# Optimization experiments

Measured on AMD Instinct MI355X. Metric: run time of the kernel, lower is better.

Reference implementation:

```python
import jax, jax.numpy as jnp
import numpy as np

N = 100000       # nodes
E = 1600000      # edges
DIM_IN = 128
DIM_H = 256
G = 512          # graphs in batch


def setup_inputs() -> dict:
    key = jax.random.key(0)
    ks = jax.random.split(key, 9)
    x = jax.random.normal(ks[0], (N, DIM_IN), dtype=jnp.float32)
    edge_index = jax.random.randint(ks[1], (2, E), 0, N, dtype=jnp.int32)
    batch = jnp.sort(jax.random.randint(ks[2], (N,), 0, G, dtype=jnp.int32))
    # GCNConv weights (glorot-ish scale) + biases, and linear head
    W1 = jax.random.normal(ks[3], (DIM_IN, DIM_H), dtype=jnp.float32) / np.sqrt(DIM_IN)
    b1 = jnp.zeros((DIM_H,), dtype=jnp.float32)
    W2 = jax.random.normal(ks[4], (DIM_H, DIM_H), dtype=jnp.float32) / np.sqrt(DIM_H)
    b2 = jnp.zeros((DIM_H,), dtype=jnp.float32)
    Wl = jax.random.normal(ks[5], (DIM_H, 1), dtype=jnp.float32) / np.sqrt(DIM_H)
    bl = jnp.zeros((1,), dtype=jnp.float32)
    return {"x": x, "edge_index": edge_index, "batch": batch,
            "W1": W1, "b1": b1, "W2": W2, "b2": b2, "Wl": Wl, "bl": bl}


def _gcn_conv(x, W, b, src, dst, norm):
    # PyG GCNConv: h = x @ W; message = norm_e * h[src]; aggregate at dst; + bias
    h = x @ W                                  # [N, d_out]
    msg = h[src] * norm[:, None]               # [E+N, d_out] edge-gathered
    out = jax.ops.segment_sum(msg, dst, num_segments=N)
    return out + b


def reference(x, edge_index, batch, W1, b1, W2, b2, Wl, bl):
    # add self-loops (PyG GCNConv default)
    loops = jnp.arange(N, dtype=edge_index.dtype)
    src = jnp.concatenate([edge_index[0], loops])   # [E+N]
    dst = jnp.concatenate([edge_index[1], loops])   # [E+N]
    # symmetric normalization: deg counted at dst (incl. self-loops)
    deg = jax.ops.segment_sum(jnp.ones_like(src, dtype=x.dtype), dst, num_segments=N)
    dinv = jax.lax.rsqrt(deg)                       # deg >= 1 due to self-loops
    norm = dinv[src] * dinv[dst]                    # [E+N]

    h = jax.nn.relu(_gcn_conv(x, W1, b1, src, dst, norm))
    h = jax.nn.relu(_gcn_conv(h, W2, b2, src, dst, norm))

    # global_mean_pool over graph ids
    sums = jax.ops.segment_sum(h, batch, num_segments=G)                  # [G, d]
    cnts = jax.ops.segment_sum(jnp.ones((N,), h.dtype), batch, num_segments=G)
    pooled = sums / jnp.maximum(cnts, 1.0)[:, None]

    return pooled @ Wl + bl                                              # [G, 1]
```

## Files before the change

kernel.cpp:

```cpp
#include <hip/hip_runtime.h>
#include <hip/hip_fp16.h>
#include <math.h>

typedef _Float16 f16x8 __attribute__((ext_vector_type(8)));
typedef float f32x4 __attribute__((ext_vector_type(4)));


__global__ void k_init(int* __restrict__ ecnt, int N) {
    int i = blockIdx.x * 256 + threadIdx.x;
    if (i < N) ecnt[i] = 0;
}

__global__ void k_edge_count(const int* __restrict__ dst, int* __restrict__ ecnt,
                             int* __restrict__ rank, int E) {
    int j = (blockIdx.x * 256 + threadIdx.x) * 2;
    if (j + 1 < E) {
        int2 d = *(const int2*)(dst + j);
        int r0 = atomicAdd(&ecnt[d.x], 1);
        int r1 = atomicAdd(&ecnt[d.y], 1);
        *(int2*)(rank + j) = make_int2(r0, r1);
    } else if (j < E) {
        rank[j] = atomicAdd(&ecnt[dst[j]], 1);
    }
}

__global__ void k_scanA(const int* __restrict__ ecnt, int* __restrict__ bsum, int N) {
    int t = threadIdx.x;
    int base = blockIdx.x * 1024;
    int s = 0;
#pragma unroll
    for (int j = 0; j < 4; ++j) {
        int i = base + j * 256 + t;
        if (i < N) s += ecnt[i];
    }
#pragma unroll
    for (int off = 32; off > 0; off >>= 1) s += __shfl_down(s, off, 64);
    __shared__ int wsum[4];
    if ((t & 63) == 0) wsum[t >> 6] = s;
    __syncthreads();
    if (t == 0) bsum[blockIdx.x] = wsum[0] + wsum[1] + wsum[2] + wsum[3];
}

__global__ void k_scanB(const int* __restrict__ bsum, int* __restrict__ boff, int NB,
                        int* __restrict__ rowstart, int N, int E) {
    __shared__ int sh[256];
    int t = threadIdx.x;
    int v = (t < NB) ? bsum[t] : 0;
    sh[t] = v;
    __syncthreads();
    for (int off = 1; off < 256; off <<= 1) {
        int u = (t >= off) ? sh[t - off] : 0;
        __syncthreads();
        sh[t] += u;
        __syncthreads();
    }
    if (t < NB) boff[t] = sh[t] - v;
    if (t == 0) rowstart[N] = E;
}

__global__ void k_scanC(const int* __restrict__ ecnt, const int* __restrict__ boff,
                        int* __restrict__ rowstart, float* __restrict__ dinv, int N) {
    int t = threadIdx.x;
    int base = blockIdx.x * 1024 + t * 4;
    int e[4];
    int s = 0;
#pragma unroll
    for (int j = 0; j < 4; ++j) {
        int i = base + j;
        e[j] = (i < N) ? ecnt[i] : 0;
        s += e[j];
    }
    __shared__ int sh[256];
    sh[t] = s;
    __syncthreads();
    for (int off = 1; off < 256; off <<= 1) {
        int u = (t >= off) ? sh[t - off] : 0;
        __syncthreads();
        sh[t] += u;
        __syncthreads();
    }
    int off0 = boff[blockIdx.x] + sh[t] - s;
    int run = 0;
#pragma unroll
    for (int j = 0; j < 4; ++j) {
        int i = base + j;
        if (i < N) {
            rowstart[i] = off0 + run;
            dinv[i] = rsqrtf((float)(e[j] + 1));
        }
        run += e[j];
    }
}

__global__ void k_scatter(const int* __restrict__ src, const int* __restrict__ dst,
                          const int* __restrict__ rowstart, const int* __restrict__ rank,
                          int* __restrict__ ssrc, int E) {
    int j = (blockIdx.x * 256 + threadIdx.x) * 4;
    if (j + 3 < E) {
        int4 s = *(const int4*)(src + j);
        int4 d = *(const int4*)(dst + j);
        int4 r = *(const int4*)(rank + j);
        ssrc[rowstart[d.x] + r.x] = s.x;
        ssrc[rowstart[d.y] + r.y] = s.y;
        ssrc[rowstart[d.z] + r.z] = s.z;
        ssrc[rowstart[d.w] + r.w] = s.w;
    } else {
        for (; j < E; ++j) ssrc[rowstart[dst[j]] + rank[j]] = src[j];
    }
}

__global__ void k_gstarts(const int* __restrict__ batch, int* __restrict__ gstart, int N, int G) {
    int i = blockIdx.x * 256 + threadIdx.x;
    if (i >= N) return;
    int bi = batch[i];
    int bp = (i == 0) ? -1 : batch[i - 1];
    for (int g = bp + 1; g <= bi; ++g) gstart[g] = i;
    if (i == N - 1) {
        for (int g = bi + 1; g <= G; ++g) gstart[g] = N;
    }
}


__global__ __launch_bounds__(256) void k_cast_f2h(const float* __restrict__ in,
                                                  __half* __restrict__ out, int n4) {
    int i = blockIdx.x * 256 + threadIdx.x;
    if (i >= n4) return;
    float4 v = *(const float4*)(in + (size_t)i * 4);
    __half2 a = __floats2half2_rn(v.x, v.y);
    __half2 b = __floats2half2_rn(v.z, v.w);
    union { __half2 h[2]; float2 f; } u;
    u.h[0] = a; u.h[1] = b;
    *(float2*)(out + (size_t)i * 4) = u.f;
}


__global__ __launch_bounds__(256) void k_wt_both(
    const float* __restrict__ W1, const float* __restrict__ W2,
    _Float16* __restrict__ W1t, _Float16* __restrict__ W2t) {
    int idx = blockIdx.x * 256 + threadIdx.x;
    if (idx < 128 * 256) {
        int c = idx >> 7, k = idx & 127;
        W1t[idx] = (_Float16)W1[k * 256 + c];
    } else if (idx < 128 * 256 + 256 * 256) {
        int j = idx - 128 * 256;
        int c = j >> 8, k = j & 255;
        W2t[j] = (_Float16)W2[k * 256 + c];
    }
}


__global__ __launch_bounds__(256) void k_agg_in(
    const _Float16* __restrict__ xh,
    const int* __restrict__ rowstart, const int* __restrict__ ssrc,
    const float* __restrict__ dinv, _Float16* __restrict__ xa_h, int N) {
    int qw = threadIdx.x >> 4;
    int l = threadIdx.x & 15;
    int v = blockIdx.x * 16 + qw;
    if (v >= N) return;
    float dv = dinv[v];
    float acc[8];
    {
        f16x8 s = *(const f16x8*)(xh + (size_t)v * 128 + l * 8);
#pragma unroll
        for (int j = 0; j < 8; ++j) acc[j] = (float)s[j] * dv;
    }
    int e = rowstart[v], e1 = rowstart[v + 1];
    for (; e + 4 <= e1; e += 4) {
        int u0 = ssrc[e], u1 = ssrc[e + 1], u2 = ssrc[e + 2], u3 = ssrc[e + 3];
        float d0 = dinv[u0], d1 = dinv[u1], d2 = dinv[u2], d3 = dinv[u3];
        f16x8 m0 = *(const f16x8*)(xh + (size_t)u0 * 128 + l * 8);
        f16x8 m1 = *(const f16x8*)(xh + (size_t)u1 * 128 + l * 8);
        f16x8 m2 = *(const f16x8*)(xh + (size_t)u2 * 128 + l * 8);
        f16x8 m3 = *(const f16x8*)(xh + (size_t)u3 * 128 + l * 8);
#pragma unroll
        for (int j = 0; j < 8; ++j) {
            acc[j] = fmaf((float)m0[j], d0, acc[j]);
            acc[j] = fmaf((float)m1[j], d1, acc[j]);
            acc[j] = fmaf((float)m2[j], d2, acc[j]);
            acc[j] = fmaf((float)m3[j], d3, acc[j]);
        }
    }
    for (; e < e1; ++e) {
        int u = ssrc[e];
        float d = dinv[u];
        f16x8 m = *(const f16x8*)(xh + (size_t)u * 128 + l * 8);
#pragma unroll
        for (int j = 0; j < 8; ++j) acc[j] = fmaf((float)m[j], d, acc[j]);
    }
    f16x8 o;
#pragma unroll
    for (int j = 0; j < 8; ++j) o[j] = (_Float16)(acc[j] * dv);
    *(f16x8*)(xa_h + (size_t)v * 128 + l * 8) = o;
}


__device__ __forceinline__ void acc_h4s(float4& acc, float2 raw) {
    union { float2 f; __half2 h[2]; } u;
    u.f = raw;
    float2 p0 = __half22float2(u.h[0]);
    float2 p1 = __half22float2(u.h[1]);
    acc.x += p0.x; acc.y += p0.y; acc.z += p1.x; acc.w += p1.y;
}

__global__ __launch_bounds__(256) void k_aggregate(
    const __half* __restrict__ hsh, const int* __restrict__ rowstart,
    const int* __restrict__ ssrc, const float* __restrict__ dinv,
    const float* __restrict__ bias, __half* __restrict__ h2h, int N) {
    int w = threadIdx.x >> 6;
    int l = threadIdx.x & 63;
    int v = blockIdx.x * 4 + w;
    if (v >= N) return;
    float4 acc = make_float4(0.f, 0.f, 0.f, 0.f);
    acc_h4s(acc, *(const float2*)(hsh + (size_t)v * 256 + l * 4));
    int e = rowstart[v], e1 = rowstart[v + 1];
    for (; e + 4 <= e1; e += 4) {
        int u0 = ssrc[e], u1 = ssrc[e + 1], u2 = ssrc[e + 2], u3 = ssrc[e + 3];
        float2 m0 = *(const float2*)(hsh + (size_t)u0 * 256 + l * 4);
        float2 m1 = *(const float2*)(hsh + (size_t)u1 * 256 + l * 4);
        float2 m2 = *(const float2*)(hsh + (size_t)u2 * 256 + l * 4);
        float2 m3 = *(const float2*)(hsh + (size_t)u3 * 256 + l * 4);
        acc_h4s(acc, m0);
        acc_h4s(acc, m1);
        acc_h4s(acc, m2);
        acc_h4s(acc, m3);
    }
    for (; e < e1; ++e) {
        int u = ssrc[e];
        acc_h4s(acc, *(const float2*)(hsh + (size_t)u * 256 + l * 4));
    }
    float d = dinv[v];
    float4 b = *(const float4*)(bias + l * 4);
    union { __half2 h[2]; float2 f; } uo;
    uo.h[0] = __floats2half2_rn(fmaxf(fmaf(acc.x, d, b.x), 0.f),
                                fmaxf(fmaf(acc.y, d, b.y), 0.f));
    uo.h[1] = __floats2half2_rn(fmaxf(fmaf(acc.z, d, b.z), 0.f),
                                fmaxf(fmaf(acc.w, d, b.w), 0.f));
    *(float2*)(h2h + (size_t)v * 256 + l * 4) = uo.f;
}


template<int K, int EPI>
__global__ __launch_bounds__(256, 2) void k_gemm_mfma(
    const _Float16* __restrict__ Ah, const _Float16* __restrict__ Wt,
    const float* __restrict__ dinv, const float* __restrict__ bias,
    _Float16* __restrict__ Ch, int Nrows, int nchunks) {
    constexpr int KS = K / 32;
    constexpr int RB = 2 * K;
    constexpr int NLD = 64 * RB / 4096;
    __shared__ _Float16 As[64 * K];

    int tid = threadIdx.x;
    int l = tid & 63;
    int wv = tid >> 6;

    int bc = wv * 64 + (l & 15);
    int bk = (l >> 4) * 8;
    f16x8 breg[4][KS];
#pragma unroll
    for (int ct = 0; ct < 4; ++ct)
#pragma unroll
        for (int ks = 0; ks < KS; ++ks)
            breg[ct][ks] = *(const f16x8*)(Wt + (size_t)(bc + ct * 16) * K + ks * 32 + bk);
    float bb[4];
    if (EPI == 1) {
#pragma unroll
        for (int ct = 0; ct < 4; ++ct) bb[ct] = bias[bc + ct * 16];
    }

    for (int ch = blockIdx.x; ch < nchunks; ch += gridDim.x) {
        int r0 = ch * 64;
#pragma unroll
        for (int i = 0; i < NLD; ++i) {
            int logical = i * 4096 + tid * 16;
            int row = logical / RB;
            int colb = (logical & (RB - 1)) ^ ((row & 7) << 4);
            int grow = r0 + row;
            grow = grow < Nrows ? grow : Nrows - 1;
            const char* src = (const char*)Ah + (size_t)grow * RB + colb;
            char* dst = (char*)As + i * 4096 + wv * 1024;
            __builtin_amdgcn_global_load_lds(
                (const __attribute__((address_space(1))) void*)src,
                (__attribute__((address_space(3))) void*)dst, 16, 0, 0);
        }
        __syncthreads();

#pragma unroll
        for (int rb = 0; rb < 4; ++rb) {
            f32x4 acc[4];
#pragma unroll
            for (int ct = 0; ct < 4; ++ct) acc[ct] = (f32x4){0.f, 0.f, 0.f, 0.f};
            int row = rb * 16 + (l & 15);
#pragma unroll
            for (int ks = 0; ks < KS; ++ks) {
                int lb = (row * RB + ks * 64 + (l >> 4) * 16) ^ ((l & 7) << 4);
                f16x8 a = *(const f16x8*)((const char*)As + lb);
#pragma unroll
                for (int ct = 0; ct < 4; ++ct)
                    acc[ct] = __builtin_amdgcn_mfma_f32_16x16x32_f16(a, breg[ct][ks], acc[ct], 0, 0, 0);
            }
            int rbase = r0 + rb * 16 + (l >> 4) * 4;
#pragma unroll
            for (int j = 0; j < 4; ++j) {
                int r = rbase + j;
                if (r < Nrows) {
                    if (EPI == 0) {
                        float sc = dinv[r];
#pragma unroll
                        for (int ct = 0; ct < 4; ++ct)
                            Ch[(size_t)r * 256 + bc + ct * 16] = (_Float16)(acc[ct][j] * sc);
                    } else {
#pragma unroll
                        for (int ct = 0; ct < 4; ++ct)
                            Ch[(size_t)r * 256 + bc + ct * 16] =
                                (_Float16)fmaxf(acc[ct][j] + bb[ct], 0.f);
                    }
                }
            }
        }
        __syncthreads();
    }
}


__global__ __launch_bounds__(256) void k_poolhead(
    const __half* __restrict__ h2h, const int* __restrict__ gstart,
    const float* __restrict__ Wl, const float* __restrict__ bl,
    float* __restrict__ out, int G) {
    int g = blockIdx.x;
    int t = threadIdx.x;
    int i0 = gstart[g], i1 = gstart[g + 1];
    float s = 0.f;
    for (int i = i0; i < i1; ++i) s += __half2float(h2h[(size_t)i * 256 + t]);
    float pooled = s / fmaxf((float)(i1 - i0), 1.f);
    float v = pooled * Wl[t];
#pragma unroll
    for (int off = 32; off > 0; off >>= 1) v += __shfl_down(v, off, 64);
    __shared__ float red[4];
    if ((t & 63) == 0) red[t >> 6] = v;
    __syncthreads();
    if (t == 0) out[g] = red[0] + red[1] + red[2] + red[3] + bl[0];
}


extern "C" void kernel_launch(void* const* d_in, const int* in_sizes, int n_in,
                              void* d_out, int out_size, void* d_ws, size_t ws_size,
                              hipStream_t stream) {
    const float* x  = (const float*)d_in[0];
    const int* ei   = (const int*)d_in[1];
    const int* batch= (const int*)d_in[2];
    const float* W1 = (const float*)d_in[3];
    const float* b1 = (const float*)d_in[4];
    const float* W2 = (const float*)d_in[5];
    const float* b2 = (const float*)d_in[6];
    const float* Wl = (const float*)d_in[7];
    const float* bl = (const float*)d_in[8];
    float* out = (float*)d_out;

    const int N = in_sizes[2];
    const int E = in_sizes[1] / 2;
    const int G = out_size;

    char* wsp = (char*)d_ws;
    size_t off = 0;
    auto carve = [&](size_t bytes) -> void* {
        void* p = wsp + off;
        off = (off + bytes + 255) & ~(size_t)255;
        return p;
    };
    float* bufA    = (float*)carve((size_t)N * 256 * 4);
    float* bufB    = (float*)carve((size_t)N * 256 * 4);
    float* dinv    = (float*)carve((size_t)N * 4);
    int* ecnt      = (int*)carve((size_t)N * 4);
    int* rowstart  = (int*)carve((size_t)(N + 1) * 4);
    int* rank      = (int*)carve((size_t)E * 4);
    int* ssrc      = (int*)carve((size_t)E * 4);
    const int NB = (N + 1023) / 1024;
    int* bsum      = (int*)carve((size_t)NB * 4);
    int* boff      = (int*)carve((size_t)NB * 4);
    int* gstart    = (int*)carve((size_t)(G + 1) * 4);
    _Float16* W1t  = (_Float16*)carve((size_t)256 * 128 * 2);
    _Float16* W2t  = (_Float16*)carve((size_t)256 * 256 * 2);
    (void)ws_size;

    _Float16* xh   = (_Float16*)bufA;
    _Float16* xa_h = (_Float16*)((char*)bufA + (size_t)N * 128 * 2);
    _Float16* h1h  = (_Float16*)((char*)bufA + (size_t)N * 128 * 4);
    _Float16* hsh  = (_Float16*)bufB;
    __half*   h2h  = (__half*)((char*)bufB + (size_t)N * 256 * 2);

    const int* esrc = ei;
    const int* edst = ei + E;

    int nb256 = (N + 255) / 256;
    int nchunks = (N + 63) / 64;

    hipLaunchKernelGGL(k_init, dim3(nb256), dim3(256), 0, stream, ecnt, N);
    hipLaunchKernelGGL(k_edge_count, dim3((E / 2 + 255) / 256), dim3(256), 0, stream,
                       edst, ecnt, rank, E);
    hipLaunchKernelGGL(k_scanA, dim3(NB), dim3(256), 0, stream, ecnt, bsum, N);
    hipLaunchKernelGGL(k_scanB, dim3(1), dim3(256), 0, stream, bsum, boff, NB, rowstart, N, E);
    hipLaunchKernelGGL(k_scanC, dim3(NB), dim3(256), 0, stream, ecnt, boff, rowstart, dinv, N);
    hipLaunchKernelGGL(k_scatter, dim3((E / 4 + 255) / 256), dim3(256), 0, stream,
                       esrc, edst, rowstart, rank, ssrc, E);
    hipLaunchKernelGGL(k_gstarts, dim3(nb256), dim3(256), 0, stream, batch, gstart, N, G);
    hipLaunchKernelGGL(k_cast_f2h, dim3((N * 32 + 255) / 256), dim3(256), 0, stream,
                       x, (__half*)xh, N * 32);
    hipLaunchKernelGGL(k_wt_both, dim3((128 * 256 + 256 * 256 + 255) / 256), dim3(256), 0, stream,
                       W1, W2, W1t, W2t);

    hipLaunchKernelGGL(k_agg_in, dim3((N + 15) / 16), dim3(256), 0, stream,
                       xh, rowstart, ssrc, dinv, xa_h, N);
    hipLaunchKernelGGL((k_gemm_mfma<128, 1>), dim3(512), dim3(256), 0, stream,
                       xa_h, W1t, (const float*)nullptr, b1, h1h, N, nchunks);
    hipLaunchKernelGGL((k_gemm_mfma<256, 0>), dim3(512), dim3(256), 0, stream,
                       h1h, W2t, dinv, (const float*)nullptr, hsh, N, nchunks);
    hipLaunchKernelGGL(k_aggregate, dim3((N + 3) / 4), dim3(256), 0, stream,
                       (const __half*)hsh, rowstart, ssrc, dinv, b2, h2h, N);
    hipLaunchKernelGGL(k_poolhead, dim3(G), dim3(256), 0, stream,
                       h2h, gstart, Wl, bl, out, G);
}
```

Before: 441.5 us.

## Fuse first-layer neighbor aggregation into GEMM1 and merge setup kernels

Neighbor aggregation for the input features is now computed directly into the GEMM's shared-memory tile, removing the intermediate aggregated buffer and its global write and read. The cast, transpose, degree-count zeroing and graph-start kernels are merged into one launch. The fused kernel runs the irregular gather inside a persistent grid of 512 blocks. This gives less latency hiding than the previous wide aggregation launch, and the GEMM phase now waits on gather completion.

```diff
diff --git a/kernel.cpp b/kernel.cpp
--- a/kernel.cpp
+++ b/kernel.cpp
@@ -5,11 +5,6 @@
 typedef _Float16 f16x8 __attribute__((ext_vector_type(8)));
 typedef float f32x4 __attribute__((ext_vector_type(4)));
 
-
-__global__ void k_init(int* __restrict__ ecnt, int N) {
-    int i = blockIdx.x * 256 + threadIdx.x;
-    if (i < N) ecnt[i] = 0;
-}
 
 __global__ void k_edge_count(const int* __restrict__ dst, int* __restrict__ ecnt,
                              int* __restrict__ rank, int E) {
@@ -109,88 +104,223 @@
     }
 }
 
-__global__ void k_gstarts(const int* __restrict__ batch, int* __restrict__ gstart, int N, int G) {
+
+__global__ __launch_bounds__(256) void k_misc(
+    const float* __restrict__ x, __half* __restrict__ xh,
+    const float* __restrict__ W1, const float* __restrict__ W2,
+    _Float16* __restrict__ W1t, _Float16* __restrict__ W2t,
+    const int* __restrict__ batch, int* __restrict__ gstart,
+    int* __restrict__ ecnt, int N, int G, int n4) {
     int i = blockIdx.x * 256 + threadIdx.x;
-    if (i >= N) return;
-    int bi = batch[i];
-    int bp = (i == 0) ? -1 : batch[i - 1];
-    for (int g = bp + 1; g <= bi; ++g) gstart[g] = i;
-    if (i == N - 1) {
-        for (int g = bi + 1; g <= G; ++g) gstart[g] = N;
-    }
-}
-
-
-__global__ __launch_bounds__(256) void k_cast_f2h(const float* __restrict__ in,
-                                                  __half* __restrict__ out, int n4) {
-    int i = blockIdx.x * 256 + threadIdx.x;
-    if (i >= n4) return;
-    float4 v = *(const float4*)(in + (size_t)i * 4);
-    __half2 a = __floats2half2_rn(v.x, v.y);
-    __half2 b = __floats2half2_rn(v.z, v.w);
-    union { __half2 h[2]; float2 f; } u;
-    u.h[0] = a; u.h[1] = b;
-    *(float2*)(out + (size_t)i * 4) = u.f;
-}
-
-
-__global__ __launch_bounds__(256) void k_wt_both(
-    const float* __restrict__ W1, const float* __restrict__ W2,
-    _Float16* __restrict__ W1t, _Float16* __restrict__ W2t) {
-    int idx = blockIdx.x * 256 + threadIdx.x;
-    if (idx < 128 * 256) {
-        int c = idx >> 7, k = idx & 127;
-        W1t[idx] = (_Float16)W1[k * 256 + c];
-    } else if (idx < 128 * 256 + 256 * 256) {
-        int j = idx - 128 * 256;
+    if (i < n4) {
+        float4 v = *(const float4*)(x + (size_t)i * 4);
+        union { __half2 h[2]; float2 f; } u;
+        u.h[0] = __floats2half2_rn(v.x, v.y);
+        u.h[1] = __floats2half2_rn(v.z, v.w);
+        *(float2*)(xh + (size_t)i * 4) = u.f;
+    }
+    if (i < N) {
+        ecnt[i] = 0;
+        int bi = batch[i];
+        int bp = (i == 0) ? -1 : batch[i - 1];
+        for (int g = bp + 1; g <= bi; ++g) gstart[g] = i;
+        if (i == N - 1) {
+            for (int g = bi + 1; g <= G; ++g) gstart[g] = N;
+        }
+    }
+    if (i < 128 * 256) {
+        int c = i >> 7, k = i & 127;
+        W1t[i] = (_Float16)W1[k * 256 + c];
+    } else if (i < 128 * 256 + 256 * 256) {
+        int j = i - 128 * 256;
         int c = j >> 8, k = j & 255;
         W2t[j] = (_Float16)W2[k * 256 + c];
     }
 }
 
 
-__global__ __launch_bounds__(256) void k_agg_in(
-    const _Float16* __restrict__ xh,
-    const int* __restrict__ rowstart, const int* __restrict__ ssrc,
-    const float* __restrict__ dinv, _Float16* __restrict__ xa_h, int N) {
-    int qw = threadIdx.x >> 4;
-    int l = threadIdx.x & 15;
-    int v = blockIdx.x * 16 + qw;
-    if (v >= N) return;
-    float dv = dinv[v];
-    float acc[8];
-    {
-        f16x8 s = *(const f16x8*)(xh + (size_t)v * 128 + l * 8);
-#pragma unroll
-        for (int j = 0; j < 8; ++j) acc[j] = (float)s[j] * dv;
-    }
-    int e = rowstart[v], e1 = rowstart[v + 1];
-    for (; e + 4 <= e1; e += 4) {
-        int u0 = ssrc[e], u1 = ssrc[e + 1], u2 = ssrc[e + 2], u3 = ssrc[e + 3];
-        float d0 = dinv[u0], d1 = dinv[u1], d2 = dinv[u2], d3 = dinv[u3];
-        f16x8 m0 = *(const f16x8*)(xh + (size_t)u0 * 128 + l * 8);
-        f16x8 m1 = *(const f16x8*)(xh + (size_t)u1 * 128 + l * 8);
-        f16x8 m2 = *(const f16x8*)(xh + (size_t)u2 * 128 + l * 8);
-        f16x8 m3 = *(const f16x8*)(xh + (size_t)u3 * 128 + l * 8);
-#pragma unroll
-        for (int j = 0; j < 8; ++j) {
-            acc[j] = fmaf((float)m0[j], d0, acc[j]);
-            acc[j] = fmaf((float)m1[j], d1, acc[j]);
-            acc[j] = fmaf((float)m2[j], d2, acc[j]);
-            acc[j] = fmaf((float)m3[j], d3, acc[j]);
-        }
-    }
-    for (; e < e1; ++e) {
-        int u = ssrc[e];
-        float d = dinv[u];
-        f16x8 m = *(const f16x8*)(xh + (size_t)u * 128 + l * 8);
-#pragma unroll
-        for (int j = 0; j < 8; ++j) acc[j] = fmaf((float)m[j], d, acc[j]);
-    }
-    f16x8 o;
-#pragma unroll
-    for (int j = 0; j < 8; ++j) o[j] = (_Float16)(acc[j] * dv);
-    *(f16x8*)(xa_h + (size_t)v * 128 + l * 8) = o;
+__global__ __launch_bounds__(256, 2) void k_agg_gemm1(
+    const _Float16* __restrict__ xh, const int* __restrict__ rowstart,
+    const int* __restrict__ ssrc, const float* __restrict__ dinv,
+    const float* __restrict__ bias, const _Float16* __restrict__ Wt,
+    _Float16* __restrict__ Ch, int Nrows, int nchunks) {
+    constexpr int K = 128, KS = K / 32, RB = 2 * K;
+    __shared__ _Float16 As[64 * K];
+
+    int tid = threadIdx.x;
+    int l = tid & 63;
+    int wv = tid >> 6;
+    int qw = tid >> 4, l16 = tid & 15;
+
+    int bc = wv * 64 + (l & 15);
+    int bk = (l >> 4) * 8;
+    f16x8 breg[4][KS];
+#pragma unroll
+    for (int ct = 0; ct < 4; ++ct)
+#pragma unroll
+        for (int ks = 0; ks < KS; ++ks)
+            breg[ct][ks] = *(const f16x8*)(Wt + (size_t)(bc + ct * 16) * K + ks * 32 + bk);
+    float bb[4];
+#pragma unroll
+    for (int ct = 0; ct < 4; ++ct) bb[ct] = bias[bc + ct * 16];
+
+    for (int ch = blockIdx.x; ch < nchunks; ch += gridDim.x) {
+        int r0 = ch * 64;
+#pragma unroll
+        for (int round = 0; round < 4; ++round) {
+            int row = round * 16 + qw;
+            int v = r0 + row;
+            float acc[8] = {0.f, 0.f, 0.f, 0.f, 0.f, 0.f, 0.f, 0.f};
+            if (v < Nrows) {
+                float dv = dinv[v];
+                f16x8 s = *(const f16x8*)(xh + (size_t)v * 128 + l16 * 8);
+#pragma unroll
+                for (int j = 0; j < 8; ++j) acc[j] = (float)s[j] * dv;
+                int e = rowstart[v], e1 = rowstart[v + 1];
+                for (; e + 4 <= e1; e += 4) {
+                    int u0 = ssrc[e], u1 = ssrc[e + 1], u2 = ssrc[e + 2], u3 = ssrc[e + 3];
+                    float d0 = dinv[u0], d1 = dinv[u1], d2 = dinv[u2], d3 = dinv[u3];
+                    f16x8 m0 = *(const f16x8*)(xh + (size_t)u0 * 128 + l16 * 8);
+                    f16x8 m1 = *(const f16x8*)(xh + (size_t)u1 * 128 + l16 * 8);
+                    f16x8 m2 = *(const f16x8*)(xh + (size_t)u2 * 128 + l16 * 8);
+                    f16x8 m3 = *(const f16x8*)(xh + (size_t)u3 * 128 + l16 * 8);
+#pragma unroll
+                    for (int j = 0; j < 8; ++j) {
+                        acc[j] = fmaf((float)m0[j], d0, acc[j]);
+                        acc[j] = fmaf((float)m1[j], d1, acc[j]);
+                        acc[j] = fmaf((float)m2[j], d2, acc[j]);
+                        acc[j] = fmaf((float)m3[j], d3, acc[j]);
+                    }
+                }
+                for (; e < e1; ++e) {
+                    int u = ssrc[e];
+                    float d = dinv[u];
+                    f16x8 m = *(const f16x8*)(xh + (size_t)u * 128 + l16 * 8);
+#pragma unroll
+                    for (int j = 0; j < 8; ++j) acc[j] = fmaf((float)m[j], d, acc[j]);
+                }
+#pragma unroll
+                for (int j = 0; j < 8; ++j) acc[j] *= dv;
+            }
+            f16x8 o;
+#pragma unroll
+            for (int j = 0; j < 8; ++j) o[j] = (_Float16)acc[j];
+            int lb = row * RB + ((l16 * 16) ^ ((row & 7) << 4));
+            *(f16x8*)((char*)As + lb) = o;
+        }
+        __syncthreads();
+
+#pragma unroll
+        for (int rb = 0; rb < 4; ++rb) {
+            f32x4 acc[4];
+#pragma unroll
+            for (int ct = 0; ct < 4; ++ct) acc[ct] = (f32x4){0.f, 0.f, 0.f, 0.f};
+            int row = rb * 16 + (l & 15);
+#pragma unroll
+            for (int ks = 0; ks < KS; ++ks) {
+                int lb = (row * RB + ks * 64 + (l >> 4) * 16) ^ ((l & 7) << 4);
+                f16x8 a = *(const f16x8*)((const char*)As + lb);
+#pragma unroll
+                for (int ct = 0; ct < 4; ++ct)
+                    acc[ct] = __builtin_amdgcn_mfma_f32_16x16x32_f16(a, breg[ct][ks], acc[ct], 0, 0, 0);
+            }
+            int rbase = r0 + rb * 16 + (l >> 4) * 4;
+#pragma unroll
+            for (int j = 0; j < 4; ++j) {
+                int r = rbase + j;
+                if (r < Nrows) {
+#pragma unroll
+                    for (int ct = 0; ct < 4; ++ct)
+                        Ch[(size_t)r * 256 + bc + ct * 16] =
+                            (_Float16)fmaxf(acc[ct][j] + bb[ct], 0.f);
+                }
+            }
+        }
+        __syncthreads();
+    }
+}
+
+
+template<int K, int EPI>
+__global__ __launch_bounds__(256, 2) void k_gemm_mfma(
+    const _Float16* __restrict__ Ah, const _Float16* __restrict__ Wt,
+    const float* __restrict__ dinv, const float* __restrict__ bias,
+    _Float16* __restrict__ Ch, int Nrows, int nchunks) {
+    constexpr int KS = K / 32;
+    constexpr int RB = 2 * K;
+    constexpr int NLD = 64 * RB / 4096;
+    __shared__ _Float16 As[64 * K];
+
+    int tid = threadIdx.x;
+    int l = tid & 63;
+    int wv = tid >> 6;
+
+    int bc = wv * 64 + (l & 15);
+    int bk = (l >> 4) * 8;
+    f16x8 breg[4][KS];
+#pragma unroll
+    for (int ct = 0; ct < 4; ++ct)
+#pragma unroll
+        for (int ks = 0; ks < KS; ++ks)
+            breg[ct][ks] = *(const f16x8*)(Wt + (size_t)(bc + ct * 16) * K + ks * 32 + bk);
+    float bb[4];
+    if (EPI == 1) {
+#pragma unroll
+        for (int ct = 0; ct < 4; ++ct) bb[ct] = bias[bc + ct * 16];
+    }
+
+    for (int ch = blockIdx.x; ch < nchunks; ch += gridDim.x) {
+        int r0 = ch * 64;
+#pragma unroll
+        for (int i = 0; i < NLD; ++i) {
+            int logical = i * 4096 + tid * 16;
+            int row = logical / RB;
+            int colb = (logical & (RB - 1)) ^ ((row & 7) << 4);
+            int grow = r0 + row;
+            grow = grow < Nrows ? grow : Nrows - 1;
+            const char* src = (const char*)Ah + (size_t)grow * RB + colb;
+            char* dst = (char*)As + i * 4096 + wv * 1024;
+            __builtin_amdgcn_global_load_lds(
+                (const __attribute__((address_space(1))) void*)src,
+                (__attribute__((address_space(3))) void*)dst, 16, 0, 0);
+        }
+        __syncthreads();
+
+#pragma unroll
+        for (int rb = 0; rb < 4; ++rb) {
+            f32x4 acc[4];
+#pragma unroll
+            for (int ct = 0; ct < 4; ++ct) acc[ct] = (f32x4){0.f, 0.f, 0.f, 0.f};
+            int row = rb * 16 + (l & 15);
+#pragma unroll
+            for (int ks = 0; ks < KS; ++ks) {
+                int lb = (row * RB + ks * 64 + (l >> 4) * 16) ^ ((l & 7) << 4);
+                f16x8 a = *(const f16x8*)((const char*)As + lb);
+#pragma unroll
+                for (int ct = 0; ct < 4; ++ct)
+                    acc[ct] = __builtin_amdgcn_mfma_f32_16x16x32_f16(a, breg[ct][ks], acc[ct], 0, 0, 0);
+            }
+            int rbase = r0 + rb * 16 + (l >> 4) * 4;
+#pragma unroll
+            for (int j = 0; j < 4; ++j) {
+                int r = rbase + j;
+                if (r < Nrows) {
+                    if (EPI == 0) {
+                        float sc = dinv[r];
+#pragma unroll
+                        for (int ct = 0; ct < 4; ++ct)
+                            Ch[(size_t)r * 256 + bc + ct * 16] = (_Float16)(acc[ct][j] * sc);
+                    } else {
+#pragma unroll
+                        for (int ct = 0; ct < 4; ++ct)
+                            Ch[(size_t)r * 256 + bc + ct * 16] =
+                                (_Float16)fmaxf(acc[ct][j] + bb[ct], 0.f);
+                    }
+                }
+            }
+        }
+        __syncthreads();
+    }
 }
 
 
@@ -239,89 +369,6 @@
 }
 
 
-template<int K, int EPI>
-__global__ __launch_bounds__(256, 2) void k_gemm_mfma(
-    const _Float16* __restrict__ Ah, const _Float16* __restrict__ Wt,
-    const float* __restrict__ dinv, const float* __restrict__ bias,
-    _Float16* __restrict__ Ch, int Nrows, int nchunks) {
-    constexpr int KS = K / 32;
-    constexpr int RB = 2 * K;
-    constexpr int NLD = 64 * RB / 4096;
-    __shared__ _Float16 As[64 * K];
-
-    int tid = threadIdx.x;
-    int l = tid & 63;
-    int wv = tid >> 6;
-
-    int bc = wv * 64 + (l & 15);
-    int bk = (l >> 4) * 8;
-    f16x8 breg[4][KS];
-#pragma unroll
-    for (int ct = 0; ct < 4; ++ct)
-#pragma unroll
-        for (int ks = 0; ks < KS; ++ks)
-            breg[ct][ks] = *(const f16x8*)(Wt + (size_t)(bc + ct * 16) * K + ks * 32 + bk);
-    float bb[4];
-    if (EPI == 1) {
-#pragma unroll
-        for (int ct = 0; ct < 4; ++ct) bb[ct] = bias[bc + ct * 16];
-    }
-
-    for (int ch = blockIdx.x; ch < nchunks; ch += gridDim.x) {
-        int r0 = ch * 64;
-#pragma unroll
-        for (int i = 0; i < NLD; ++i) {
-            int logical = i * 4096 + tid * 16;
-            int row = logical / RB;
-            int colb = (logical & (RB - 1)) ^ ((row & 7) << 4);
-            int grow = r0 + row;
-            grow = grow < Nrows ? grow : Nrows - 1;
-            const char* src = (const char*)Ah + (size_t)grow * RB + colb;
-            char* dst = (char*)As + i * 4096 + wv * 1024;
-            __builtin_amdgcn_global_load_lds(
-                (const __attribute__((address_space(1))) void*)src,
-                (__attribute__((address_space(3))) void*)dst, 16, 0, 0);
-        }
-        __syncthreads();
-
-#pragma unroll
-        for (int rb = 0; rb < 4; ++rb) {
-            f32x4 acc[4];
-#pragma unroll
-            for (int ct = 0; ct < 4; ++ct) acc[ct] = (f32x4){0.f, 0.f, 0.f, 0.f};
-            int row = rb * 16 + (l & 15);
-#pragma unroll
-            for (int ks = 0; ks < KS; ++ks) {
-                int lb = (row * RB + ks * 64 + (l >> 4) * 16) ^ ((l & 7) << 4);
-                f16x8 a = *(const f16x8*)((const char*)As + lb);
-#pragma unroll
-                for (int ct = 0; ct < 4; ++ct)
-                    acc[ct] = __builtin_amdgcn_mfma_f32_16x16x32_f16(a, breg[ct][ks], acc[ct], 0, 0, 0);
-            }
-            int rbase = r0 + rb * 16 + (l >> 4) * 4;
-#pragma unroll
-            for (int j = 0; j < 4; ++j) {
-                int r = rbase + j;
-                if (r < Nrows) {
-                    if (EPI == 0) {
-                        float sc = dinv[r];
-#pragma unroll
-                        for (int ct = 0; ct < 4; ++ct)
-                            Ch[(size_t)r * 256 + bc + ct * 16] = (_Float16)(acc[ct][j] * sc);
-                    } else {
-#pragma unroll
-                        for (int ct = 0; ct < 4; ++ct)
-                            Ch[(size_t)r * 256 + bc + ct * 16] =
-                                (_Float16)fmaxf(acc[ct][j] + bb[ct], 0.f);
-                    }
-                }
-            }
-        }
-        __syncthreads();
-    }
-}
-
-
 __global__ __launch_bounds__(256) void k_poolhead(
     const __half* __restrict__ h2h, const int* __restrict__ gstart,
     const float* __restrict__ Wl, const float* __restrict__ bl,
@@ -383,7 +430,6 @@
     (void)ws_size;
 
     _Float16* xh   = (_Float16*)bufA;
-    _Float16* xa_h = (_Float16*)((char*)bufA + (size_t)N * 128 * 2);
     _Float16* h1h  = (_Float16*)((char*)bufA + (size_t)N * 128 * 4);
     _Float16* hsh  = (_Float16*)bufB;
     __half*   h2h  = (__half*)((char*)bufB + (size_t)N * 256 * 2);
@@ -391,10 +437,11 @@
     const int* esrc = ei;
     const int* edst = ei + E;
 
-    int nb256 = (N + 255) / 256;
     int nchunks = (N + 63) / 64;
-
-    hipLaunchKernelGGL(k_init, dim3(nb256), dim3(256), 0, stream, ecnt, N);
+    int n4 = N * 32;
+
+    hipLaunchKernelGGL(k_misc, dim3((n4 + 255) / 256), dim3(256), 0, stream,
+                       x, (__half*)xh, W1, W2, W1t, W2t, batch, gstart, ecnt, N, G, n4);
     hipLaunchKernelGGL(k_edge_count, dim3((E / 2 + 255) / 256), dim3(256), 0, stream,
                        edst, ecnt, rank, E);
     hipLaunchKernelGGL(k_scanA, dim3(NB), dim3(256), 0, stream, ecnt, bsum, N);
@@ -402,16 +449,9 @@
     hipLaunchKernelGGL(k_scanC, dim3(NB), dim3(256), 0, stream, ecnt, boff, rowstart, dinv, N);
     hipLaunchKernelGGL(k_scatter, dim3((E / 4 + 255) / 256), dim3(256), 0, stream,
                        esrc, edst, rowstart, rank, ssrc, E);
-    hipLaunchKernelGGL(k_gstarts, dim3(nb256), dim3(256), 0, stream, batch, gstart, N, G);
-    hipLaunchKernelGGL(k_cast_f2h, dim3((N * 32 + 255) / 256), dim3(256), 0, stream,
-                       x, (__half*)xh, N * 32);
-    hipLaunchKernelGGL(k_wt_both, dim3((128 * 256 + 256 * 256 + 255) / 256), dim3(256), 0, stream,
-                       W1, W2, W1t, W2t);
-
-    hipLaunchKernelGGL(k_agg_in, dim3((N + 15) / 16), dim3(256), 0, stream,
-                       xh, rowstart, ssrc, dinv, xa_h, N);
-    hipLaunchKernelGGL((k_gemm_mfma<128, 1>), dim3(512), dim3(256), 0, stream,
-                       xa_h, W1t, (const float*)nullptr, b1, h1h, N, nchunks);
+
+    hipLaunchKernelGGL(k_agg_gemm1, dim3(512), dim3(256), 0, stream,
+                       xh, rowstart, ssrc, dinv, b1, W1t, h1h, N, nchunks);
     hipLaunchKernelGGL((k_gemm_mfma<256, 0>), dim3(512), dim3(256), 0, stream,
                        h1h, W2t, dinv, (const float*)nullptr, hsh, N, nchunks);
     hipLaunchKernelGGL(k_aggregate, dim3((N + 3) / 4), dim3(256), 0, stream,
```

New measurement: 445.2 us. About the same (+0.8%).

## Fuse setup kernels and partition scatter by destination range across block classes

Applied to the files above, without the earlier changes.

Four small setup kernels (counter zeroing, the x cast to half, weight transposes, graph starts) are merged into one launch to cut launch overhead. The edge scatter becomes a grid-stride kernel in which blocks form eight classes, each writing only edges whose destination falls in its node range. This is meant to keep each class's scattered writes within a narrower region of ssrc for better cache and write locality. The cost is that every class re-reads all of src, dst and rank, eight times the read traffic. The GEMM kernel is only moved within the file.

```diff
diff --git a/kernel.cpp b/kernel.cpp
--- a/kernel.cpp
+++ b/kernel.cpp
@@ -5,11 +5,6 @@
 typedef _Float16 f16x8 __attribute__((ext_vector_type(8)));
 typedef float f32x4 __attribute__((ext_vector_type(4)));
 
-
-__global__ void k_init(int* __restrict__ ecnt, int N) {
-    int i = blockIdx.x * 256 + threadIdx.x;
-    if (i < N) ecnt[i] = 0;
-}
 
 __global__ void k_edge_count(const int* __restrict__ dst, int* __restrict__ ecnt,
                              int* __restrict__ rank, int E) {
@@ -92,57 +87,63 @@
     }
 }
 
-__global__ void k_scatter(const int* __restrict__ src, const int* __restrict__ dst,
-                          const int* __restrict__ rowstart, const int* __restrict__ rank,
-                          int* __restrict__ ssrc, int E) {
-    int j = (blockIdx.x * 256 + threadIdx.x) * 4;
-    if (j + 3 < E) {
-        int4 s = *(const int4*)(src + j);
-        int4 d = *(const int4*)(dst + j);
-        int4 r = *(const int4*)(rank + j);
-        ssrc[rowstart[d.x] + r.x] = s.x;
-        ssrc[rowstart[d.y] + r.y] = s.y;
-        ssrc[rowstart[d.z] + r.z] = s.z;
-        ssrc[rowstart[d.w] + r.w] = s.w;
-    } else {
-        for (; j < E; ++j) ssrc[rowstart[dst[j]] + rank[j]] = src[j];
-    }
-}
-
-__global__ void k_gstarts(const int* __restrict__ batch, int* __restrict__ gstart, int N, int G) {
+__global__ __launch_bounds__(256) void k_scatter8(
+    const int* __restrict__ src, const int* __restrict__ dst,
+    const int* __restrict__ rowstart, const int* __restrict__ rank,
+    int* __restrict__ ssrc, int E, int lo_div) {
+    int cls = blockIdx.x & 7;
+    int blk = blockIdx.x >> 3;
+    int nblk = gridDim.x >> 3;
+    int lo = cls * lo_div, hi = lo + lo_div;
+    int nchunk = (E + 1023) / 1024;
+    for (int ch = blk; ch < nchunk; ch += nblk) {
+        int j = ch * 1024 + threadIdx.x * 4;
+        if (j + 3 < E) {
+            int4 d = *(const int4*)(dst + j);
+            int4 s = *(const int4*)(src + j);
+            int4 r = *(const int4*)(rank + j);
+            if (d.x >= lo && d.x < hi) ssrc[rowstart[d.x] + r.x] = s.x;
+            if (d.y >= lo && d.y < hi) ssrc[rowstart[d.y] + r.y] = s.y;
+            if (d.z >= lo && d.z < hi) ssrc[rowstart[d.z] + r.z] = s.z;
+            if (d.w >= lo && d.w < hi) ssrc[rowstart[d.w] + r.w] = s.w;
+        } else {
+            for (; j < E; ++j) {
+                int dv = dst[j];
+                if (dv >= lo && dv < hi) ssrc[rowstart[dv] + rank[j]] = src[j];
+            }
+        }
+    }
+}
+
+
+__global__ __launch_bounds__(256) void k_misc(
+    const float* __restrict__ x, __half* __restrict__ xh,
+    const float* __restrict__ W1, const float* __restrict__ W2,
+    _Float16* __restrict__ W1t, _Float16* __restrict__ W2t,
+    const int* __restrict__ batch, int* __restrict__ gstart,
+    int* __restrict__ ecnt, int N, int G, int n4) {
     int i = blockIdx.x * 256 + threadIdx.x;
-    if (i >= N) return;
-    int bi = batch[i];
-    int bp = (i == 0) ? -1 : batch[i - 1];
-    for (int g = bp + 1; g <= bi; ++g) gstart[g] = i;
-    if (i == N - 1) {
-        for (int g = bi + 1; g <= G; ++g) gstart[g] = N;
-    }
-}
-
-
-__global__ __launch_bounds__(256) void k_cast_f2h(const float* __restrict__ in,
-                                                  __half* __restrict__ out, int n4) {
-    int i = blockIdx.x * 256 + threadIdx.x;
-    if (i >= n4) return;
-    float4 v = *(const float4*)(in + (size_t)i * 4);
-    __half2 a = __floats2half2_rn(v.x, v.y);
-    __half2 b = __floats2half2_rn(v.z, v.w);
-    union { __half2 h[2]; float2 f; } u;
-    u.h[0] = a; u.h[1] = b;
-    *(float2*)(out + (size_t)i * 4) = u.f;
-}
-
-
-__global__ __launch_bounds__(256) void k_wt_both(
-    const float* __restrict__ W1, const float* __restrict__ W2,
-    _Float16* __restrict__ W1t, _Float16* __restrict__ W2t) {
-    int idx = blockIdx.x * 256 + threadIdx.x;
-    if (idx < 128 * 256) {
-        int c = idx >> 7, k = idx & 127;
-        W1t[idx] = (_Float16)W1[k * 256 + c];
-    } else if (idx < 128 * 256 + 256 * 256) {
-        int j = idx - 128 * 256;
+    if (i < n4) {
+        float4 v = *(const float4*)(x + (size_t)i * 4);
+        union { __half2 h[2]; float2 f; } u;
+        u.h[0] = __floats2half2_rn(v.x, v.y);
+        u.h[1] = __floats2half2_rn(v.z, v.w);
+        *(float2*)(xh + (size_t)i * 4) = u.f;
+    }
+    if (i < N) {
+        ecnt[i] = 0;
+        int bi = batch[i];
+        int bp = (i == 0) ? -1 : batch[i - 1];
+        for (int g = bp + 1; g <= bi; ++g) gstart[g] = i;
+        if (i == N - 1) {
+            for (int g = bi + 1; g <= G; ++g) gstart[g] = N;
+        }
+    }
+    if (i < 128 * 256) {
+        int c = i >> 7, k = i & 127;
+        W1t[i] = (_Float16)W1[k * 256 + c];
+    } else if (i < 128 * 256 + 256 * 256) {
+        int j = i - 128 * 256;
         int c = j >> 8, k = j & 255;
         W2t[j] = (_Float16)W2[k * 256 + c];
     }
@@ -191,6 +192,89 @@
 #pragma unroll
     for (int j = 0; j < 8; ++j) o[j] = (_Float16)(acc[j] * dv);
     *(f16x8*)(xa_h + (size_t)v * 128 + l * 8) = o;
+}
+
+
+template<int K, int EPI>
+__global__ __launch_bounds__(256, 2) void k_gemm_mfma(
+    const _Float16* __restrict__ Ah, const _Float16* __restrict__ Wt,
+    const float* __restrict__ dinv, const float* __restrict__ bias,
+    _Float16* __restrict__ Ch, int Nrows, int nchunks) {
+    constexpr int KS = K / 32;
+    constexpr int RB = 2 * K;
+    constexpr int NLD = 64 * RB / 4096;
+    __shared__ _Float16 As[64 * K];
+
+    int tid = threadIdx.x;
+    int l = tid & 63;
+    int wv = tid >> 6;
+
+    int bc = wv * 64 + (l & 15);
+    int bk = (l >> 4) * 8;
+    f16x8 breg[4][KS];
+#pragma unroll
+    for (int ct = 0; ct < 4; ++ct)
+#pragma unroll
+        for (int ks = 0; ks < KS; ++ks)
+            breg[ct][ks] = *(const f16x8*)(Wt + (size_t)(bc + ct * 16) * K + ks * 32 + bk);
+    float bb[4];
+    if (EPI == 1) {
+#pragma unroll
+        for (int ct = 0; ct < 4; ++ct) bb[ct] = bias[bc + ct * 16];
+    }
+
+    for (int ch = blockIdx.x; ch < nchunks; ch += gridDim.x) {
+        int r0 = ch * 64;
+#pragma unroll
+        for (int i = 0; i < NLD; ++i) {
+            int logical = i * 4096 + tid * 16;
+            int row = logical / RB;
+            int colb = (logical & (RB - 1)) ^ ((row & 7) << 4);
+            int grow = r0 + row;
+            grow = grow < Nrows ? grow : Nrows - 1;
+            const char* src = (const char*)Ah + (size_t)grow * RB + colb;
+            char* dst = (char*)As + i * 4096 + wv * 1024;
+            __builtin_amdgcn_global_load_lds(
+                (const __attribute__((address_space(1))) void*)src,
+                (__attribute__((address_space(3))) void*)dst, 16, 0, 0);
+        }
+        __syncthreads();
+
+#pragma unroll
+        for (int rb = 0; rb < 4; ++rb) {
+            f32x4 acc[4];
+#pragma unroll
+            for (int ct = 0; ct < 4; ++ct) acc[ct] = (f32x4){0.f, 0.f, 0.f, 0.f};
+            int row = rb * 16 + (l & 15);
+#pragma unroll
+            for (int ks = 0; ks < KS; ++ks) {
+                int lb = (row * RB + ks * 64 + (l >> 4) * 16) ^ ((l & 7) << 4);
+                f16x8 a = *(const f16x8*)((const char*)As + lb);
+#pragma unroll
+                for (int ct = 0; ct < 4; ++ct)
+                    acc[ct] = __builtin_amdgcn_mfma_f32_16x16x32_f16(a, breg[ct][ks], acc[ct], 0, 0, 0);
+            }
+            int rbase = r0 + rb * 16 + (l >> 4) * 4;
+#pragma unroll
+            for (int j = 0; j < 4; ++j) {
+                int r = rbase + j;
+                if (r < Nrows) {
+                    if (EPI == 0) {
+                        float sc = dinv[r];
+#pragma unroll
+                        for (int ct = 0; ct < 4; ++ct)
+                            Ch[(size_t)r * 256 + bc + ct * 16] = (_Float16)(acc[ct][j] * sc);
+                    } else {
+#pragma unroll
+                        for (int ct = 0; ct < 4; ++ct)
+                            Ch[(size_t)r * 256 + bc + ct * 16] =
+                                (_Float16)fmaxf(acc[ct][j] + bb[ct], 0.f);
+                    }
+                }
+            }
+        }
+        __syncthreads();
+    }
 }
 
 
@@ -239,89 +323,6 @@
 }
 
 
-template<int K, int EPI>
-__global__ __launch_bounds__(256, 2) void k_gemm_mfma(
-    const _Float16* __restrict__ Ah, const _Float16* __restrict__ Wt,
-    const float* __restrict__ dinv, const float* __restrict__ bias,
-    _Float16* __restrict__ Ch, int Nrows, int nchunks) {
-    constexpr int KS = K / 32;
-    constexpr int RB = 2 * K;
-    constexpr int NLD = 64 * RB / 4096;
-    __shared__ _Float16 As[64 * K];
-
-    int tid = threadIdx.x;
-    int l = tid & 63;
-    int wv = tid >> 6;
-
-    int bc = wv * 64 + (l & 15);
-    int bk = (l >> 4) * 8;
-    f16x8 breg[4][KS];
-#pragma unroll
-    for (int ct = 0; ct < 4; ++ct)
-#pragma unroll
-        for (int ks = 0; ks < KS; ++ks)
-            breg[ct][ks] = *(const f16x8*)(Wt + (size_t)(bc + ct * 16) * K + ks * 32 + bk);
-    float bb[4];
-    if (EPI == 1) {
-#pragma unroll
-        for (int ct = 0; ct < 4; ++ct) bb[ct] = bias[bc + ct * 16];
-    }
-
-    for (int ch = blockIdx.x; ch < nchunks; ch += gridDim.x) {
-        int r0 = ch * 64;
-#pragma unroll
-        for (int i = 0; i < NLD; ++i) {
-            int logical = i * 4096 + tid * 16;
-            int row = logical / RB;
-            int colb = (logical & (RB - 1)) ^ ((row & 7) << 4);
-            int grow = r0 + row;
-            grow = grow < Nrows ? grow : Nrows - 1;
-            const char* src = (const char*)Ah + (size_t)grow * RB + colb;
-            char* dst = (char*)As + i * 4096 + wv * 1024;
-            __builtin_amdgcn_global_load_lds(
-                (const __attribute__((address_space(1))) void*)src,
-                (__attribute__((address_space(3))) void*)dst, 16, 0, 0);
-        }
-        __syncthreads();
-
-#pragma unroll
-        for (int rb = 0; rb < 4; ++rb) {
-            f32x4 acc[4];
-#pragma unroll
-            for (int ct = 0; ct < 4; ++ct) acc[ct] = (f32x4){0.f, 0.f, 0.f, 0.f};
-            int row = rb * 16 + (l & 15);
-#pragma unroll
-            for (int ks = 0; ks < KS; ++ks) {
-                int lb = (row * RB + ks * 64 + (l >> 4) * 16) ^ ((l & 7) << 4);
-                f16x8 a = *(const f16x8*)((const char*)As + lb);
-#pragma unroll
-                for (int ct = 0; ct < 4; ++ct)
-                    acc[ct] = __builtin_amdgcn_mfma_f32_16x16x32_f16(a, breg[ct][ks], acc[ct], 0, 0, 0);
-            }
-            int rbase = r0 + rb * 16 + (l >> 4) * 4;
-#pragma unroll
-            for (int j = 0; j < 4; ++j) {
-                int r = rbase + j;
-                if (r < Nrows) {
-                    if (EPI == 0) {
-                        float sc = dinv[r];
-#pragma unroll
-                        for (int ct = 0; ct < 4; ++ct)
-                            Ch[(size_t)r * 256 + bc + ct * 16] = (_Float16)(acc[ct][j] * sc);
-                    } else {
-#pragma unroll
-                        for (int ct = 0; ct < 4; ++ct)
-                            Ch[(size_t)r * 256 + bc + ct * 16] =
-                                (_Float16)fmaxf(acc[ct][j] + bb[ct], 0.f);
-                    }
-                }
-            }
-        }
-        __syncthreads();
-    }
-}
-
-
 __global__ __launch_bounds__(256) void k_poolhead(
     const __half* __restrict__ h2h, const int* __restrict__ gstart,
     const float* __restrict__ Wl, const float* __restrict__ bl,
@@ -391,22 +392,19 @@
     const int* esrc = ei;
     const int* edst = ei + E;
 
-    int nb256 = (N + 255) / 256;
     int nchunks = (N + 63) / 64;
-
-    hipLaunchKernelGGL(k_init, dim3(nb256), dim3(256), 0, stream, ecnt, N);
+    int n4 = N * 32;
+    int lo_div = (N + 7) / 8;
+
+    hipLaunchKernelGGL(k_misc, dim3((n4 + 255) / 256), dim3(256), 0, stream,
+                       x, (__half*)xh, W1, W2, W1t, W2t, batch, gstart, ecnt, N, G, n4);
     hipLaunchKernelGGL(k_edge_count, dim3((E / 2 + 255) / 256), dim3(256), 0, stream,
                        edst, ecnt, rank, E);
     hipLaunchKernelGGL(k_scanA, dim3(NB), dim3(256), 0, stream, ecnt, bsum, N);
     hipLaunchKernelGGL(k_scanB, dim3(1), dim3(256), 0, stream, bsum, boff, NB, rowstart, N, E);
     hipLaunchKernelGGL(k_scanC, dim3(NB), dim3(256), 0, stream, ecnt, boff, rowstart, dinv, N);
-    hipLaunchKernelGGL(k_scatter, dim3((E / 4 + 255) / 256), dim3(256), 0, stream,
-                       esrc, edst, rowstart, rank, ssrc, E);
-    hipLaunchKernelGGL(k_gstarts, dim3(nb256), dim3(256), 0, stream, batch, gstart, N, G);
-    hipLaunchKernelGGL(k_cast_f2h, dim3((N * 32 + 255) / 256), dim3(256), 0, stream,
-                       x, (__half*)xh, N * 32);
-    hipLaunchKernelGGL(k_wt_both, dim3((128 * 256 + 256 * 256 + 255) / 256), dim3(256), 0, stream,
-                       W1, W2, W1t, W2t);
+    hipLaunchKernelGGL(k_scatter8, dim3(2048), dim3(256), 0, stream,
+                       esrc, edst, rowstart, rank, ssrc, E, lo_div);
 
     hipLaunchKernelGGL(k_agg_in, dim3((N + 15) / 16), dim3(256), 0, stream,
                        xh, rowstart, ssrc, dinv, xa_h, N);
```

Result: faster. 423.3 us, median of 2 (-4.1%).
